# Performance work log

Measured on AMD Instinct MI355X. Metric: run time of the kernel, lower is better.

## Reference

```python
import jax, jax.numpy as jnp
import numpy as np

B, S, IN, OUT = 4, 2048, 4096, 16384

def setup_inputs() -> dict:
    key = jax.random.key(0)
    k1, k2, k3, k4 = jax.random.split(key, 4)
    x = jax.random.normal(k1, (B, S, IN), dtype=jnp.float32)
    quantized_weight = jax.random.randint(k2, (OUT, IN), 0, 16, dtype=jnp.int32)
    scale = jax.random.uniform(k3, (OUT,), dtype=jnp.float32)
    zero_point = jax.random.randint(k4, (OUT,), 0, 16, dtype=jnp.int32)
    return {"x": x, "quantized_weight": quantized_weight, "scale": scale, "zero_point": zero_point}

def reference(x, quantized_weight, scale, zero_point):
    # Per-output-channel dequantization: W = (q - zp) * scale, shape [OUT, IN]
    weight = (quantized_weight.astype(jnp.float32) - zero_point.astype(jnp.float32)[:, None]) * scale[:, None]
    # F.linear(x, W) = x @ W.T -> [B, S, OUT]
    return jnp.einsum('bsi,oi->bso', x, weight)
```

## Files before the change

kernel.cpp:

```cpp
#include <hip/hip_runtime.h>
#include <stdint.h>

#define MDIM 8192
#define NDIM 16384
#define KDIM 4096
#define NT   64

typedef __attribute__((ext_vector_type(4))) int i32x4;

__device__ __forceinline__ void gload_lds16(const void* g, void* l) {
    __builtin_amdgcn_global_load_lds(
        (const __attribute__((address_space(1))) void*)g,
        (__attribute__((address_space(3))) void*)l,
        16, 0, 0);
}

__device__ __forceinline__ i32x4 MFMA8(i32x4 a, i32x4 b, i32x4 c) {
    return __builtin_amdgcn_mfma_i32_16x16x64_i8(a, b, c, 0, 0, 0);
}


__global__ __launch_bounds__(256)
void quant_x_kernel(const float* __restrict__ x, int8_t* __restrict__ xq,
                    float* __restrict__ sx) {
    const int row = (int)blockIdx.x;
    const float* xr = x + (long)row * KDIM;
    const int t = threadIdx.x;
    float v[16];
#pragma unroll
    for (int i = 0; i < 4; ++i)
        *(float4*)&v[i * 4] = ((const float4*)xr)[t + 256 * i];
    float m = 0.f;
#pragma unroll
    for (int i = 0; i < 16; ++i) m = fmaxf(m, fabsf(v[i]));
#pragma unroll
    for (int off = 32; off >= 1; off >>= 1) m = fmaxf(m, __shfl_xor(m, off));
    __shared__ float red[4];
    if ((t & 63) == 0) red[t >> 6] = m;
    __syncthreads();
    m = fmaxf(fmaxf(red[0], red[1]), fmaxf(red[2], red[3]));
    m = fmaxf(m, 1e-20f);
    const float inv = 127.0f / m;
    if (t == 0) sx[row] = m * (1.0f / 127.0f);
    int* qo = (int*)(xq + (long)row * KDIM);
#pragma unroll
    for (int i = 0; i < 4; ++i) {
        union { int8_t c[4]; int w; } o;
#pragma unroll
        for (int j = 0; j < 4; ++j)
            o.c[j] = (int8_t)__float2int_rn(v[i * 4 + j] * inv);
        qo[t + 256 * i] = o.w;
    }
}

__global__ __launch_bounds__(256)
void quant_w_kernel(const int* __restrict__ q, const int* __restrict__ zp,
                    int8_t* __restrict__ wq) {
    const long i = (long)blockIdx.x * 256 + threadIdx.x;
    const long e = i * 16;
    const int o = (int)(e >> 12);
    const int z = zp[o];
    union { int8_t c[16]; int4 v; } r;
#pragma unroll
    for (int b = 0; b < 4; ++b) {
        int4 a = ((const int4*)(q + e))[b];
        r.c[b * 4 + 0] = (int8_t)(a.x - z);
        r.c[b * 4 + 1] = (int8_t)(a.y - z);
        r.c[b * 4 + 2] = (int8_t)(a.z - z);
        r.c[b * 4 + 3] = (int8_t)(a.w - z);
    }
    *(int4*)(wq + e) = r.v;
}


__global__ __launch_bounds__(512, 2)
void gemm_i8_kernel(const int8_t* __restrict__ A, const int8_t* __restrict__ Wt,
                    const float* __restrict__ scale, const float* __restrict__ sx,
                    float* __restrict__ C) {
    __shared__ int8_t lds[3 * 32768];

    const int wg = (int)blockIdx.x;
    const int rr = wg >> 8;
    const int ii = wg & 255;
    const int bm = ii & 31;
    const int bn = rr * 8 + (ii >> 5);

    const int tid  = threadIdx.x;
    const int lane = tid & 63;
    const int wid  = tid >> 6;
    const int wm   = wid >> 2;
    const int wn   = wid & 3;
    const int l15  = lane & 15;
    const int c16  = lane >> 4;

    const int axor = (l15 >> 1) & 3;
    const int fro  = l15 * 64 + ((c16 ^ axor) << 4);

    const int soff = (tid >> 2) * KDIM + ((((tid & 3) ^ ((tid >> 3) & 3))) << 4);
    const int dl   = tid * 16;

    const int8_t* Ab  = A  + (long)bm * 256 * KDIM;
    const int8_t* Wb  = Wt + (long)bn * 256 * KDIM;
    const int8_t* Ab2 = Ab + (long)128 * KDIM;
    const int8_t* Wb2 = Wb + (long)128 * KDIM;

#define STG(DSTB, SRC, TT) gload_lds16((SRC) + soff + (TT) * 64, &lds[(DSTB) + dl])

#define RDA(DST, BB, IB)                                                            \
    _Pragma("unroll")                                                               \
    for (int i_ = 0; i_ < 4; ++i_)                                                  \
        DST[i_] = *(const i32x4*)&lds[(BB) + (wm * 128 + ((IB) + i_) * 16) * 64 + fro];

#define RDB2(DST, BB, JB)                                                           \
    _Pragma("unroll")                                                               \
    for (int j_ = 0; j_ < 2; ++j_)                                                  \
        DST[j_] = *(const i32x4*)&lds[(BB) + 16384 + (wn * 64 + ((JB) + j_) * 16) * 64 + fro];

#define MFQ(IB, JB, AS, BS)                                                         \
    do {                                                                            \
        __builtin_amdgcn_sched_barrier(0);                                          \
        __builtin_amdgcn_s_setprio(1);                                              \
        _Pragma("unroll")                                                           \
        for (int i_ = 0; i_ < 4; ++i_)                                              \
            _Pragma("unroll")                                                       \
            for (int j_ = 0; j_ < 2; ++j_)                                          \
                acc[(IB) + i_][(JB) + j_] =                                         \
                    MFMA8(AS[i_], BS[j_], acc[(IB) + i_][(JB) + j_]);               \
        __builtin_amdgcn_s_setprio(0);                                              \
        __builtin_amdgcn_sched_barrier(0);                                          \
    } while (0)

    i32x4 acc[8][4];
#pragma unroll
    for (int i = 0; i < 8; ++i)
#pragma unroll
        for (int j = 0; j < 4; ++j) acc[i][j] = (i32x4){0, 0, 0, 0};

    i32x4 aLo[4], aHi[4], bLo[2], bHi[2];

    int cb = 0, nb = 32768, fb = 65536;

    STG(cb + 0, Ab, 0); STG(cb + 16384, Wb, 0); STG(cb + 8192, Ab2, 0); STG(cb + 24576, Wb2, 0);
    STG(nb + 0, Ab, 1); STG(nb + 16384, Wb, 1); STG(nb + 8192, Ab2, 1); STG(nb + 24576, Wb2, 1);
    asm volatile("s_waitcnt vmcnt(4)" ::: "memory");
    __builtin_amdgcn_s_barrier();

    for (int t = 0; t < NT; ++t) {
        const int tt = (t + 2 < NT) ? (t + 2) : (NT - 1);

        RDA(aLo, cb, 0);
        RDB2(bLo, cb, 0);
        STG(fb + 0, Ab, tt);
        __builtin_amdgcn_s_barrier();
        asm volatile("s_waitcnt lgkmcnt(0)" ::: "memory");
        MFQ(0, 0, aLo, bLo);

        RDA(aHi, cb, 4);
        STG(fb + 16384, Wb, tt);
        __builtin_amdgcn_s_barrier();
        asm volatile("s_waitcnt lgkmcnt(0)" ::: "memory");
        MFQ(4, 0, aHi, bLo);

        RDB2(bHi, cb, 2);
        STG(fb + 8192, Ab2, tt);
        __builtin_amdgcn_s_barrier();
        asm volatile("s_waitcnt lgkmcnt(0)" ::: "memory");
        MFQ(0, 2, aLo, bHi);

        STG(fb + 24576, Wb2, tt);
        asm volatile("s_waitcnt vmcnt(4)" ::: "memory");
        __builtin_amdgcn_s_barrier();
        MFQ(4, 2, aHi, bHi);

        const int tb = cb; cb = nb; nb = fb; fb = tb;
    }
#undef STG
#undef RDA
#undef RDB2
#undef MFQ

    const long rowA0 = (long)bm * 256 + wm * 128;
    const int  colB0 = bn * 256 + wn * 64;
    float scj[4];
#pragma unroll
    for (int j = 0; j < 4; ++j) scj[j] = scale[colB0 + j * 16 + l15];
#pragma unroll
    for (int i = 0; i < 8; ++i) {
        const long rbase = rowA0 + i * 16 + c16 * 4;
        const float4 s4 = *(const float4*)(sx + rbase);
#pragma unroll
        for (int j = 0; j < 4; ++j) {
            float* cp = C + rbase * NDIM + colB0 + j * 16 + l15;
            cp[0 * (long)NDIM] = (float)acc[i][j][0] * scj[j] * s4.x;
            cp[1 * (long)NDIM] = (float)acc[i][j][1] * scj[j] * s4.y;
            cp[2 * (long)NDIM] = (float)acc[i][j][2] * scj[j] * s4.z;
            cp[3 * (long)NDIM] = (float)acc[i][j][3] * scj[j] * s4.w;
        }
    }
}


__global__ __launch_bounds__(256)
void fallback_kernel(const float* __restrict__ x, const int* __restrict__ q,
                     const float* __restrict__ scale, const int* __restrict__ zp,
                     float* __restrict__ out) {
    __shared__ float sA[64][17];
    __shared__ float sB[64][17];
    const int bn = (int)blockIdx.x % (NDIM / 64);
    const int bm = (int)blockIdx.x / (NDIM / 64);
    const int t  = threadIdx.x;
    const int tx = t & 15, ty = t >> 4;
    const long rowA = (long)bm * 64, rowB = (long)bn * 64;
    float acc[4][4] = {};
    for (int k0 = 0; k0 < KDIM; k0 += 16) {
#pragma unroll
        for (int i = 0; i < 4; ++i) {
            const int e = t + i * 256;
            const int r = e >> 4, c = e & 15;
            sA[r][c] = x[(rowA + r) * KDIM + k0 + c];
            const int o = (int)rowB + r;
            sB[r][c] = (float)(q[(long)o * KDIM + k0 + c] - zp[o]) * scale[o];
        }
        __syncthreads();
#pragma unroll
        for (int kk = 0; kk < 16; ++kk) {
            float a[4], b[4];
#pragma unroll
            for (int i = 0; i < 4; ++i) a[i] = sA[ty * 4 + i][kk];
#pragma unroll
            for (int j = 0; j < 4; ++j) b[j] = sB[tx * 4 + j][kk];
#pragma unroll
            for (int i = 0; i < 4; ++i)
#pragma unroll
                for (int j = 0; j < 4; ++j) acc[i][j] += a[i] * b[j];
        }
        __syncthreads();
    }
#pragma unroll
    for (int i = 0; i < 4; ++i) {
        const long r = rowA + ty * 4 + i;
#pragma unroll
        for (int j = 0; j < 4; ++j)
            out[r * NDIM + rowB + tx * 4 + j] = acc[i][j];
    }
}


extern "C" void kernel_launch(void* const* d_in, const int* in_sizes, int n_in,
                              void* d_out, int out_size, void* d_ws, size_t ws_size,
                              hipStream_t stream) {
    const float* x     = (const float*)d_in[0];
    const int*   qw    = (const int*)d_in[1];
    const float* scale = (const float*)d_in[2];
    const int*   zp    = (const int*)d_in[3];
    float*       out   = (float*)d_out;

    const size_t needA  = (size_t)MDIM * KDIM;
    const size_t needW  = (size_t)NDIM * KDIM;
    const size_t needSx = (size_t)MDIM * sizeof(float);

    if (ws_size >= needA + needW + needSx) {
        int8_t* xq = (int8_t*)d_ws;
        int8_t* wq = xq + needA;
        float*  sx = (float*)((char*)d_ws + needA + needW);
        quant_x_kernel<<<MDIM, 256, 0, stream>>>(x, xq, sx);
        quant_w_kernel<<<(NDIM * (KDIM / 16)) / 256, 256, 0, stream>>>(qw, zp, wq);
        gemm_i8_kernel<<<(MDIM / 256) * (NDIM / 256), 512, 0, stream>>>(xq, wq, scale, sx, out);
    } else {
        fallback_kernel<<<(MDIM / 64) * (NDIM / 64), 256, 0, stream>>>(x, qw, scale, zp, out);
    }
}
```

Measured before the change: 678.6 us.

## Deepen int8 GEMM to 4-stage LDS pipeline with register-prefetched fragments

```diff
diff --git a/kernel.cpp b/kernel.cpp
--- a/kernel.cpp
+++ b/kernel.cpp
@@ -77,7 +77,7 @@
 void gemm_i8_kernel(const int8_t* __restrict__ A, const int8_t* __restrict__ Wt,
                     const float* __restrict__ scale, const float* __restrict__ sx,
                     float* __restrict__ C) {
-    __shared__ int8_t lds[3 * 32768];
+    extern __shared__ int8_t lds[];
 
     const int wg = (int)blockIdx.x;
     const int rr = wg >> 8;
@@ -106,7 +106,7 @@
 
 #define STG(DSTB, SRC, TT) gload_lds16((SRC) + soff + (TT) * 64, &lds[(DSTB) + dl])
 
-#define RDA(DST, BB, IB)                                                            \
+#define RDA4(DST, BB, IB)                                                           \
     _Pragma("unroll")                                                               \
     for (int i_ = 0; i_ < 4; ++i_)                                                  \
         DST[i_] = *(const i32x4*)&lds[(BB) + (wm * 128 + ((IB) + i_) * 16) * 64 + fro];
@@ -130,52 +130,63 @@
         __builtin_amdgcn_sched_barrier(0);                                          \
     } while (0)
 
+#define TILE(T, ACUR, BCUR, ANXT, BNXT)                                             \
+    do {                                                                            \
+             \
+        RDA4(aHi, b0, 4);                                                           \
+        asm volatile("s_waitcnt lgkmcnt(4)" ::: "memory");                          \
+        MFQ(0, 0, ACUR, BCUR);                                                      \
+                                                             \
+        RDB2(bHi, b0, 2);                                                           \
+        asm volatile("s_waitcnt lgkmcnt(2)" ::: "memory");                          \
+        MFQ(4, 0, aHi, BCUR);                                                       \
+                                        \
+        if ((T) < NT - 1) {                                                         \
+            RDA4(ANXT, b1, 0);                                                      \
+            RDB2(BNXT, b1, 0);                                                      \
+            asm volatile("s_waitcnt lgkmcnt(6)" ::: "memory");                      \
+        } else {                                                                    \
+            asm volatile("s_waitcnt lgkmcnt(0)" ::: "memory");                      \
+        }                                                                           \
+        MFQ(0, 2, ACUR, bHi);                                                       \
+                    \
+        {                                                                           \
+            const int tt = ((T) + 3 < NT) ? ((T) + 3) : (NT - 1);                   \
+            STG(b3 + 0, Ab, tt);  STG(b3 + 16384, Wb, tt);                          \
+            STG(b3 + 8192, Ab2, tt); STG(b3 + 24576, Wb2, tt);                      \
+        }                                                                           \
+        asm volatile("s_waitcnt vmcnt(4)" ::: "memory");                            \
+        __builtin_amdgcn_s_barrier();                                               \
+        MFQ(4, 2, aHi, bHi);                                                        \
+        { const int tb = b0; b0 = b1; b1 = b2; b2 = b3; b3 = tb; }                  \
+    } while (0)
+
     i32x4 acc[8][4];
 #pragma unroll
     for (int i = 0; i < 8; ++i)
 #pragma unroll
         for (int j = 0; j < 4; ++j) acc[i][j] = (i32x4){0, 0, 0, 0};
 
-    i32x4 aLo[4], aHi[4], bLo[2], bHi[2];
-
-    int cb = 0, nb = 32768, fb = 65536;
-
-    STG(cb + 0, Ab, 0); STG(cb + 16384, Wb, 0); STG(cb + 8192, Ab2, 0); STG(cb + 24576, Wb2, 0);
-    STG(nb + 0, Ab, 1); STG(nb + 16384, Wb, 1); STG(nb + 8192, Ab2, 1); STG(nb + 24576, Wb2, 1);
+    i32x4 aLoA[4], aLoB[4], aHi[4];
+    i32x4 bLoA[2], bLoB[2], bHi[2];
+
+    int b0 = 0, b1 = 32768, b2 = 65536, b3 = 98304;
+
+    STG(b0 + 0, Ab, 0); STG(b0 + 16384, Wb, 0); STG(b0 + 8192, Ab2, 0); STG(b0 + 24576, Wb2, 0);
+    STG(b1 + 0, Ab, 1); STG(b1 + 16384, Wb, 1); STG(b1 + 8192, Ab2, 1); STG(b1 + 24576, Wb2, 1);
+    STG(b2 + 0, Ab, 2); STG(b2 + 16384, Wb, 2); STG(b2 + 8192, Ab2, 2); STG(b2 + 24576, Wb2, 2);
     asm volatile("s_waitcnt vmcnt(4)" ::: "memory");
     __builtin_amdgcn_s_barrier();
-
-    for (int t = 0; t < NT; ++t) {
-        const int tt = (t + 2 < NT) ? (t + 2) : (NT - 1);
-
-        RDA(aLo, cb, 0);
-        RDB2(bLo, cb, 0);
-        STG(fb + 0, Ab, tt);
-        __builtin_amdgcn_s_barrier();
-        asm volatile("s_waitcnt lgkmcnt(0)" ::: "memory");
-        MFQ(0, 0, aLo, bLo);
-
-        RDA(aHi, cb, 4);
-        STG(fb + 16384, Wb, tt);
-        __builtin_amdgcn_s_barrier();
-        asm volatile("s_waitcnt lgkmcnt(0)" ::: "memory");
-        MFQ(4, 0, aHi, bLo);
-
-        RDB2(bHi, cb, 2);
-        STG(fb + 8192, Ab2, tt);
-        __builtin_amdgcn_s_barrier();
-        asm volatile("s_waitcnt lgkmcnt(0)" ::: "memory");
-        MFQ(0, 2, aLo, bHi);
-
-        STG(fb + 24576, Wb2, tt);
-        asm volatile("s_waitcnt vmcnt(4)" ::: "memory");
-        __builtin_amdgcn_s_barrier();
-        MFQ(4, 2, aHi, bHi);
-
-        const int tb = cb; cb = nb; nb = fb; fb = tb;
-    }
+    RDA4(aLoA, b0, 0);
+    RDB2(bLoA, b0, 0);
+
+    for (int t = 0; t < NT; t += 2) {
+        TILE(t,     aLoA, bLoA, aLoB, bLoB);
+        TILE(t + 1, aLoB, bLoB, aLoA, bLoA);
+    }
+#undef TILE
 #undef STG
-#undef RDA
+#undef RDA4
 #undef RDB2
 #undef MFQ
 
@@ -265,7 +276,9 @@
         float*  sx = (float*)((char*)d_ws + needA + needW);
         quant_x_kernel<<<MDIM, 256, 0, stream>>>(x, xq, sx);
         quant_w_kernel<<<(NDIM * (KDIM / 16)) / 256, 256, 0, stream>>>(qw, zp, wq);
-        gemm_i8_kernel<<<(MDIM / 256) * (NDIM / 256), 512, 0, stream>>>(xq, wq, scale, sx, out);
+        (void)hipFuncSetAttribute((const void*)gemm_i8_kernel,
+                                  hipFuncAttributeMaxDynamicSharedMemorySize, 131072);
+        gemm_i8_kernel<<<(MDIM / 256) * (NDIM / 256), 512, 131072, stream>>>(xq, wq, scale, sx, out);
     } else {
         fallback_kernel<<<(MDIM / 64) * (NDIM / 64), 256, 0, stream>>>(x, qw, scale, zp, out);
     }
```

After: 700.9 us. 3.3% more time.
